# Kernel tuning notes

Measured on AMD Instinct MI355X. Metric: run time of the kernel, lower is better.

## Reference

```python
import jax, jax.numpy as jnp
import numpy as np

BLOCK = 128
FP8_MAX = 448.0  # max representable value of float8_e4m3fn
F8 = jnp.float8_e4m3fn


def setup_inputs() -> dict:
    key = jax.random.key(0)
    k1, k2, k3 = jax.random.split(key, 3)
    M, K, N = 4096, 7168, 16384
    x = jax.random.normal(k1, (M, K), jnp.float32)
    w = jax.random.normal(k2, (N, K), jnp.float32)  # raw weight; cast to fp8 in reference to simulate stored fp8
    w_scale = jax.random.uniform(k3, (N // BLOCK, K // BLOCK), jnp.float32, 0.5, 1.5)
    return {"x": x, "w": w, "w_scale": w_scale, "block_size": BLOCK}


def act_quant(x, b):
    M, K = x.shape
    xb = x.reshape(M, K // b, b)
    s = jnp.max(jnp.abs(xb), axis=-1) / FP8_MAX  # [M, K//b]
    xq = (xb / s[..., None]).astype(F8).astype(jnp.float32).reshape(M, K)
    return xq, s


def reference(x, w, w_scale, block_size):
    b = block_size
    # simulate fp8-stored weight (element_size == 1 branch)
    w8 = w.astype(F8).astype(jnp.float32)  # [N, K]
    # fp8_gemm: y[m,n] = sum_k xq[m,k]*w8[n,k]*xs[m,kb]*ws[nb,kb]
    # scales factor per-element, so dequantize both operands then one dense GEMM
    xq, xs = act_quant(x, b)
    x_dq = xq * jnp.repeat(xs, b, axis=1)                         # [M, K]
    w_dq = w8 * jnp.repeat(jnp.repeat(w_scale, b, axis=0), b, axis=1)  # [N, K]
    return x_dq @ w_dq.T  # [M, N], no bias (bias=False)
```

## Files before the change

kernel.cpp:

```cpp
#include <hip/hip_runtime.h>
#include <hip/hip_bf16.h>
#include <hip/hip_fp8.h>

typedef __attribute__((ext_vector_type(4))) float f32x4;
typedef __attribute__((ext_vector_type(2))) long long ll2;

#define AS1 __attribute__((address_space(1)))
#define AS3 __attribute__((address_space(3)))

static constexpr int Mdim = 4096;
static constexpr int Kdim = 7168;
static constexpr int Ndim = 16384;
static constexpr int KB   = Kdim / 128;
static constexpr float FP8_MAX = 448.0f;

#define BARRIER() do { asm volatile("" ::: "memory"); \
                       __builtin_amdgcn_s_barrier();  \
                       asm volatile("" ::: "memory"); } while (0)

#define MFMA_FP8 __builtin_amdgcn_mfma_f32_16x16x32_fp8_fp8

__global__ __launch_bounds__(256) void quant_x_kernel(
    const float* __restrict__ x, unsigned char* __restrict__ xq,
    float* __restrict__ xst)
{
    constexpr int NBLK = Mdim * KB;
    const int lane = threadIdx.x & 63;
    const int wid  = (blockIdx.x * 256 + threadIdx.x) >> 6;
    const int nw   = (gridDim.x * 256) >> 6;

    for (int b = wid; b < NBLK; b += nw) {
        size_t base = (size_t)b * 128 + lane * 2;
        float2 v = *reinterpret_cast<const float2*>(x + base);
        float amax = fmaxf(fabsf(v.x), fabsf(v.y));
#pragma unroll
        for (int off = 32; off > 0; off >>= 1)
            amax = fmaxf(amax, __shfl_xor(amax, off));
        float s = amax * (1.0f / FP8_MAX);
        unsigned char q0 = 0, q1 = 0;
        if (s > 0.0f) {
            q0 = __hip_fp8_e4m3(v.x / s).__x;
            q1 = __hip_fp8_e4m3(v.y / s).__x;
        }
        *reinterpret_cast<unsigned short*>(xq + base) =
            (unsigned short)(q0 | ((unsigned short)q1 << 8));
        if (lane == 0) {
            int row = b / KB, kb = b - row * KB;
            xst[(size_t)kb * Mdim + row] = s;
        }
    }
}

__global__ __launch_bounds__(256) void quant_w_kernel(
    const float* __restrict__ w, unsigned char* __restrict__ w8)
{
    constexpr size_t NCHUNK = (size_t)Ndim * Kdim / 8;

    size_t idx    = (size_t)blockIdx.x * 256 + threadIdx.x;
    size_t stride = (size_t)gridDim.x * 256;

    for (size_t c = idx; c < NCHUNK; c += stride) {
        const float* src = w + c * 8;
        float4 v0 = *reinterpret_cast<const float4*>(src);
        float4 v1 = *reinterpret_cast<const float4*>(src + 4);
        unsigned int lo = (unsigned int)__hip_fp8_e4m3(v0.x).__x
                        | ((unsigned int)__hip_fp8_e4m3(v0.y).__x << 8)
                        | ((unsigned int)__hip_fp8_e4m3(v0.z).__x << 16)
                        | ((unsigned int)__hip_fp8_e4m3(v0.w).__x << 24);
        unsigned int hi = (unsigned int)__hip_fp8_e4m3(v1.x).__x
                        | ((unsigned int)__hip_fp8_e4m3(v1.y).__x << 8)
                        | ((unsigned int)__hip_fp8_e4m3(v1.z).__x << 16)
                        | ((unsigned int)__hip_fp8_e4m3(v1.w).__x << 24);
        uint2 p; p.x = lo; p.y = hi;
        *reinterpret_cast<uint2*>(w8 + c * 8) = p;
    }
}

constexpr int BM = 128, BN = 256, BK = 64;
constexpr int NT  = Kdim / BK;
constexpr int NBN = Ndim / BN;
constexpr int NWG = (Mdim / BM) * NBN;
constexpr int K1  = Kdim;
constexpr int BUFSZ  = 24576;
constexpr int XS_OFF = 49152;
constexpr int WS_OFF = XS_OFF + 56 * 512;
constexpr int LDS_TOT = WS_OFF + 448;

__global__ __launch_bounds__(512, 2) void gemm128_fp8_kernel(
    const unsigned char* __restrict__ Ag,
    const unsigned char* __restrict__ Bg,
    const float* __restrict__ xsT,
    const float* __restrict__ Wsc,
    float* __restrict__ C)
{
    extern __shared__ char smem[];

    const int tid  = threadIdx.x;
    const int w    = tid >> 6;
    const int lane = tid & 63;
    const int wr   = w >> 2;
    const int wc   = w & 3;
    const int lr   = lane & 15;
    const int lk   = lane >> 4;

    int bid = (int)blockIdx.x;
    int swz = (bid & 7) * (NWG >> 3) + (bid >> 3);
    const int bm = (swz / NBN) * BM;
    const int bn = (swz % NBN) * BN;

    const int colF = (lk ^ ((lr >> 1) & 3)) << 4;
    const int aRow = wr * 64;
    const int bRow = (wc & 1) * 64;

    const char* xsL0 = smem + XS_OFF + (wr * 64 + lk * 4) * 4;
    const char* wsL  = smem + WS_OFF + (wc >> 1) * (KB * 4);

    const int rowS = tid >> 2;
    const int colS = (((tid & 3) ^ ((rowS >> 1) & 3))) * 16;
    const size_t offG = (size_t)rowS * K1 + colS;
    const int ldsW = w * 1024;

    const char* Ab = (const char*)Ag + (size_t)bm * K1;
    const char* Bb = (const char*)Bg + (size_t)bn * K1;

    auto stage = [&](int T, int r) {
        if (T >= NT) return;
        const int regByte = (T & 1) * BUFSZ + r * 8192;
        const char* g = (r ? Bb + (size_t)(r - 1) * (128 * (size_t)K1) : Ab)
                        + (size_t)T * 64 + offG;
        __builtin_amdgcn_global_load_lds((const AS1 void*)g,
                                         (AS3 void*)(smem + regByte + ldsW),
                                         16, 0, 0);
    };

#pragma unroll
    for (int i = 0; i < 4; ++i) {
        const int c = i * 8 + w;
        if (c < 28) {
            const int kb  = 2 * c + (lane >> 5);
            const int row = (lane & 31) * 4;
            const float* g = xsT + (size_t)kb * Mdim + bm + row;
            __builtin_amdgcn_global_load_lds((const AS1 void*)g,
                (AS3 void*)(smem + XS_OFF + c * 1024), 16, 0, 0);
        }
    }
    if (w == 0 && lane < 28) {
        const float* g = Wsc + (size_t)(bn >> 7) * KB + lane * 4;
        __builtin_amdgcn_global_load_lds((const AS1 void*)g,
            (AS3 void*)(smem + WS_OFF), 16, 0, 0);
    }
    stage(0, 0); stage(0, 1); stage(0, 2);
    stage(1, 1); stage(1, 2);
    asm volatile("s_waitcnt vmcnt(2)" ::: "memory");
    BARRIER();

    f32x4 acc[4][4] = {};

    for (int t = 0; t < NT; ++t) {
        const int buf = t & 1;
        const int kb  = t >> 1;
        const char* aB = smem + buf * BUFSZ;
        const char* bB = smem + buf * BUFSZ + 8192 + (wc >> 1) * 8192;
        ll2 a[4], b0[2], b1[2];
        f32x4 sv[4];

        const float wsv  = *(const float*)(wsL + kb * 4);
        const char* xsLk = xsL0 + kb * 512;

        stage(t + 1, 0);
#pragma unroll
        for (int m = 0; m < 4; ++m)
            a[m] = *(const ll2*)(aB + (aRow + m * 16 + lr) * 64 + colF);
#pragma unroll
        for (int n = 0; n < 2; ++n)
            b0[n] = *(const ll2*)(bB + (bRow + n * 16 + lr) * 64 + colF);
#pragma unroll
        for (int n = 0; n < 2; ++n)
            b1[n] = *(const ll2*)(bB + (bRow + (n + 2) * 16 + lr) * 64 + colF);
#pragma unroll
        for (int m = 0; m < 4; ++m)
            sv[m] = *reinterpret_cast<const f32x4*>(xsLk + m * 64) * wsv;
        __builtin_amdgcn_s_setprio(1);
#pragma unroll
        for (int m = 0; m < 4; ++m)
#pragma unroll
            for (int n = 0; n < 2; ++n) {
                f32x4 pacc = {0.f, 0.f, 0.f, 0.f};
                pacc = MFMA_FP8(a[m][0], b0[n][0], pacc, 0, 0, 0);
                pacc = MFMA_FP8(a[m][1], b0[n][1], pacc, 0, 0, 0);
                acc[m][n] += sv[m] * pacc;
            }
        __builtin_amdgcn_s_setprio(0);
        asm volatile("s_waitcnt lgkmcnt(0)" ::: "memory");
        BARRIER();

        stage(t + 2, 1);
        stage(t + 2, 2);
        __builtin_amdgcn_s_setprio(1);
#pragma unroll
        for (int m = 0; m < 4; ++m)
#pragma unroll
            for (int n = 0; n < 2; ++n) {
                f32x4 pacc = {0.f, 0.f, 0.f, 0.f};
                pacc = MFMA_FP8(a[m][0], b1[n][0], pacc, 0, 0, 0);
                pacc = MFMA_FP8(a[m][1], b1[n][1], pacc, 0, 0, 0);
                acc[m][n + 2] += sv[m] * pacc;
            }
        __builtin_amdgcn_s_setprio(0);
        if (t < NT - 2) { asm volatile("s_waitcnt vmcnt(2)" ::: "memory"); }
        else            { asm volatile("s_waitcnt vmcnt(0)" ::: "memory"); }
        BARRIER();
    }

#pragma unroll
    for (int m = 0; m < 4; ++m) {
#pragma unroll
        for (int n = 0; n < 4; ++n) {
            const int row0 = bm + wr * 64 + m * 16 + lk * 4;
            const int col  = bn + wc * 64 + n * 16 + lr;
#pragma unroll
            for (int j = 0; j < 4; ++j)
                C[(size_t)(row0 + j) * Ndim + col] = acc[m][n][j];
        }
    }
}

extern "C" void kernel_launch(void* const* d_in, const int* in_sizes, int n_in,
                              void* d_out, int out_size, void* d_ws, size_t ws_size,
                              hipStream_t stream) {
    const float* x  = (const float*)d_in[0];
    const float* w  = (const float*)d_in[1];
    const float* ws = (const float*)d_in[2];

    unsigned char* xq  = (unsigned char*)d_ws;
    unsigned char* w8  = xq + (size_t)Mdim * Kdim;
    float*         xst = (float*)(w8 + (size_t)Ndim * Kdim);

    quant_x_kernel<<<2048, 256, 0, stream>>>(x, xq, xst);
    quant_w_kernel<<<4096, 256, 0, stream>>>(w, w8);

    hipFuncSetAttribute((const void*)gemm128_fp8_kernel,
                        hipFuncAttributeMaxDynamicSharedMemorySize, LDS_TOT);
    gemm128_fp8_kernel<<<NWG, 512, LDS_TOT, stream>>>(xq, w8, xst, ws,
                                                      (float*)d_out);
}
```

Measured before the change: 1.067 ms.

## Grow FP8 GEMM tile to 256x256 with 1024-thread workgroups

Doubles the M tile from 128 to 256 and uses 16 waves per workgroup so each wave owns a 64x64 output patch. A and B stages become single 16KB loads per thread-sweep, and the activation-scale table is enlarged for 256 rows. This raises arithmetic intensity per byte loaded from global memory and halves the number of workgroups. In exchange, roughly 123KB of LDS likely limits residency to one workgroup per CU, and the tighter launch bounds may cap registers.

```diff
diff --git a/kernel.cpp b/kernel.cpp
--- a/kernel.cpp
+++ b/kernel.cpp
@@ -76,17 +76,17 @@
     }
 }
 
-constexpr int BM = 128, BN = 256, BK = 64;
+constexpr int BM = 256, BN = 256, BK = 64;
 constexpr int NT  = Kdim / BK;
 constexpr int NBN = Ndim / BN;
 constexpr int NWG = (Mdim / BM) * NBN;
 constexpr int K1  = Kdim;
-constexpr int BUFSZ  = 24576;
-constexpr int XS_OFF = 49152;
-constexpr int WS_OFF = XS_OFF + 56 * 512;
+constexpr int BUFSZ  = 32768;
+constexpr int XS_OFF = 65536;
+constexpr int WS_OFF = XS_OFF + 56 * 1024;
 constexpr int LDS_TOT = WS_OFF + 448;
 
-__global__ __launch_bounds__(512, 2) void gemm128_fp8_kernel(
+__global__ __launch_bounds__(1024, 4) void gemm256_fp8_kernel(
     const unsigned char* __restrict__ Ag,
     const unsigned char* __restrict__ Bg,
     const float* __restrict__ xsT,
@@ -110,7 +110,7 @@
 
     const int colF = (lk ^ ((lr >> 1) & 3)) << 4;
     const int aRow = wr * 64;
-    const int bRow = (wc & 1) * 64;
+    const int bRow = wc * 64;
 
     const char* xsL0 = smem + XS_OFF + (wr * 64 + lk * 4) * 4;
     const char* wsL  = smem + WS_OFF + (wc >> 1) * (KB * 4);
@@ -123,11 +123,10 @@
     const char* Ab = (const char*)Ag + (size_t)bm * K1;
     const char* Bb = (const char*)Bg + (size_t)bn * K1;
 
-    auto stage = [&](int T, int r) {
+    auto stage = [&](int T, int isB) {
         if (T >= NT) return;
-        const int regByte = (T & 1) * BUFSZ + r * 8192;
-        const char* g = (r ? Bb + (size_t)(r - 1) * (128 * (size_t)K1) : Ab)
-                        + (size_t)T * 64 + offG;
+        const int regByte = (T & 1) * BUFSZ + isB * 16384;
+        const char* g = (isB ? Bb : Ab) + (size_t)T * 64 + offG;
         __builtin_amdgcn_global_load_lds((const AS1 void*)g,
                                          (AS3 void*)(smem + regByte + ldsW),
                                          16, 0, 0);
@@ -135,13 +134,13 @@
 
 #pragma unroll
     for (int i = 0; i < 4; ++i) {
-        const int c = i * 8 + w;
-        if (c < 28) {
-            const int kb  = 2 * c + (lane >> 5);
-            const int row = (lane & 31) * 4;
-            const float* g = xsT + (size_t)kb * Mdim + bm + row;
+        const int c = i * 1024 + tid;
+        if (c < 56 * 64) {
+            const int kb2 = c >> 6;
+            const int row = (c & 63) * 4;
+            const float* g = xsT + (size_t)kb2 * Mdim + bm + row;
             __builtin_amdgcn_global_load_lds((const AS1 void*)g,
-                (AS3 void*)(smem + XS_OFF + c * 1024), 16, 0, 0);
+                (AS3 void*)(smem + XS_OFF + i * 16384 + ldsW), 16, 0, 0);
         }
     }
     if (w == 0 && lane < 28) {
@@ -149,9 +148,8 @@
         __builtin_amdgcn_global_load_lds((const AS1 void*)g,
             (AS3 void*)(smem + WS_OFF), 16, 0, 0);
     }
-    stage(0, 0); stage(0, 1); stage(0, 2);
-    stage(1, 1); stage(1, 2);
-    asm volatile("s_waitcnt vmcnt(2)" ::: "memory");
+    stage(0, 0); stage(0, 1); stage(1, 1);
+    asm volatile("s_waitcnt vmcnt(1)" ::: "memory");
     BARRIER();
 
     f32x4 acc[4][4] = {};
@@ -160,12 +158,12 @@
         const int buf = t & 1;
         const int kb  = t >> 1;
         const char* aB = smem + buf * BUFSZ;
-        const char* bB = smem + buf * BUFSZ + 8192 + (wc >> 1) * 8192;
+        const char* bB = smem + buf * BUFSZ + 16384;
         ll2 a[4], b0[2], b1[2];
         f32x4 sv[4];
 
         const float wsv  = *(const float*)(wsL + kb * 4);
-        const char* xsLk = xsL0 + kb * 512;
+        const char* xsLk = xsL0 + (kb << 10);
 
         stage(t + 1, 0);
 #pragma unroll
@@ -195,7 +193,6 @@
         BARRIER();
 
         stage(t + 2, 1);
-        stage(t + 2, 2);
         __builtin_amdgcn_s_setprio(1);
 #pragma unroll
         for (int m = 0; m < 4; ++m)
@@ -207,7 +204,7 @@
                 acc[m][n + 2] += sv[m] * pacc;
             }
         __builtin_amdgcn_s_setprio(0);
-        if (t < NT - 2) { asm volatile("s_waitcnt vmcnt(2)" ::: "memory"); }
+        if (t < NT - 2) { asm volatile("s_waitcnt vmcnt(1)" ::: "memory"); }
         else            { asm volatile("s_waitcnt vmcnt(0)" ::: "memory"); }
         BARRIER();
     }
@@ -239,8 +236,8 @@
     quant_x_kernel<<<2048, 256, 0, stream>>>(x, xq, xst);
     quant_w_kernel<<<4096, 256, 0, stream>>>(w, w8);
 
-    hipFuncSetAttribute((const void*)gemm128_fp8_kernel,
+    hipFuncSetAttribute((const void*)gemm256_fp8_kernel,
                         hipFuncAttributeMaxDynamicSharedMemorySize, LDS_TOT);
-    gemm128_fp8_kernel<<<NWG, 512, LDS_TOT, stream>>>(xq, w8, xst, ws,
-                                                      (float*)d_out);
-}
+    gemm256_fp8_kernel<<<NWG, 1024, LDS_TOT, stream>>>(xq, w8, xst, ws,
+                                                       (float*)d_out);
+}
```

Result: no change. 1.059 ms (-0.8%).
